# Optimization experiments

Hardware: AMD Instinct MI355X
Metric: run time of the kernel (lower is better)

Reference implementation:

```python
import jax, jax.numpy as jnp
import numpy as np

B, N, M = 2, 4096, 12288
K, SH, H, GK, NC, F = 64, 32, 64, 8, 200, 1


def sph_to_cart(theta, phi):
    st = jnp.sin(theta)
    return jnp.stack([st * jnp.cos(phi), st * jnp.sin(phi), jnp.cos(theta)], axis=-1)


def setup_inputs() -> dict:
    key = jax.random.key(0)
    ks = jax.random.split(key, 16)
    theta = jax.random.uniform(ks[0], (B, N)) * jnp.pi
    phi = jax.random.uniform(ks[1], (B, N)) * 2 * jnp.pi
    feat = jax.random.normal(ks[2], (B, N))
    xxx = jnp.stack([theta, phi, feat], axis=1)  # [B,3,N]
    pt = jax.random.uniform(ks[3], (M,)) * jnp.pi
    pp = jax.random.uniform(ks[4], (M,)) * 2 * jnp.pi
    pix_theta_phi = jnp.stack([pt, pp], axis=1)  # [M,2]
    s = 0.1
    return dict(
        xxx=xxx,
        pix_theta_phi=pix_theta_phi,
        att_w1=jax.random.normal(ks[5], (F + 1, SH)) * s,
        att_b1=jnp.zeros((SH,)),
        att_w2=jax.random.normal(ks[6], (SH, 1)) * s,
        att_b2=jnp.zeros((1,)),
        proj_w=jax.random.normal(ks[7], (F, H)) * s,
        proj_b=jnp.zeros((H,)),
        rel_w=jax.random.normal(ks[8], (3, H, H)) * s,
        rel_b=jnp.zeros((3, H)),
        root_w=jax.random.normal(ks[9], (3, H, H)) * s,
        out_w1=jax.random.normal(ks[10], (H, H)) * s,
        out_b1=jnp.zeros((H,)),
        out_w2=jax.random.normal(ks[11], (H, NC)) * s,
        out_b2=jnp.zeros((NC,)),
    )


def reference(xxx, pix_theta_phi, att_w1, att_b1, att_w2, att_b2, proj_w, proj_b,
              rel_w, rel_b, root_w, out_w1, out_b1, out_w2, out_b2):
    # --- sparse healpix sampler ---
    los_tp = jnp.transpose(xxx[:, :2, :], (0, 2, 1))   # [B,N,2]
    x = xxx[:, 2, :][..., None]                        # [B,N,1]
    r_los = sph_to_cart(los_tp[..., 0], los_tp[..., 1])           # [B,N,3]
    r_pix = sph_to_cart(pix_theta_phi[:, 0], pix_theta_phi[:, 1])  # [M,3]
    cos = jnp.clip(jnp.einsum('bnc,mc->bmn', r_los, r_pix), -1.0, 1.0)  # [B,M,N]
    vals, idx = jax.lax.top_k(cos, K)                  # [B,M,K]
    x_g = jax.vmap(lambda xb, ib: xb[ib])(x, idx)      # [B,M,K,F]
    d = jnp.arccos(jnp.clip(vals, -1.0, 1.0))          # [B,M,K]
    feat = jnp.concatenate([x_g, d[..., None]], axis=-1)  # [B,M,K,F+1]
    logits = jax.nn.relu(feat @ att_w1 + att_b1) @ att_w2 + att_b2  # [B,M,K,1]
    w = jax.nn.softmax(logits[..., 0], axis=-1)        # [B,M,K]
    pooled = jnp.einsum('bmk,bmkf->bmf', w, x_g)       # [B,M,F]
    # --- GNN on healpix grid ---
    h = jax.nn.relu(pooled @ proj_w + proj_b)          # [B,M,H]
    m = r_pix.shape[0]
    sq = jnp.sum(r_pix * r_pix, axis=1)
    d2 = sq[:, None] + sq[None, :] - 2.0 * (r_pix @ r_pix.T)       # [M,M]
    d2 = jnp.where(jnp.eye(m, dtype=bool), jnp.inf, d2)  # loop=False
    _, nbr = jax.lax.top_k(-d2, GK)                    # [M,GK] knn_graph
    for i in range(rel_w.shape[0]):
        agg = h[:, nbr, :].sum(axis=2)                 # sum-aggregate neighbor msgs
        h = jax.nn.relu(agg @ rel_w[i] + rel_b[i] + h @ root_w[i])
    graph_feat = h.mean(axis=1)                        # global_mean_pool -> [B,H]
    out = jax.nn.relu(graph_feat @ out_w1 + out_b1) @ out_w2 + out_b2
    return out
```

## Files before the change

### kernel.cpp

```cpp
#include <hip/hip_runtime.h>
#include <hip/hip_bf16.h>

#define B_ 2
#define N_ 4096
#define M_ 12288
#define K_ 64
#define SH_ 32
#define H_ 64
#define GK_ 8
#define NC_ 200

#define KCAP 128
#define BCAP2 48
#define MG_ 0.01f
#define C256_ 81.48733086f

static __device__ __forceinline__ unsigned f2key(float f) {
  unsigned b = __float_as_uint(f);
  return (b & 0x80000000u) ? ~b : (b | 0x80000000u);
}
static __device__ __forceinline__ float key2f(unsigned u) {
  unsigned b = (u & 0x80000000u) ? (u & 0x7fffffffu) : ~u;
  return __uint_as_float(b);
}
static __device__ __forceinline__ unsigned long long shflxor64(unsigned long long x, int m) {
  unsigned lo = (unsigned)x, hi = (unsigned)(x >> 32);
  lo = (unsigned)__shfl_xor((int)lo, m);
  hi = (unsigned)__shfl_xor((int)hi, m);
  return ((unsigned long long)hi << 32) | lo;
}
static __device__ __forceinline__ unsigned long long kpack(float s, int j) {
  return ((unsigned long long)f2key(s) << 14) | (unsigned)(16383 - j);
}
static __device__ __forceinline__ unsigned long long spack(float c, int n) {
  return ((unsigned long long)f2key(c) << 12) | (unsigned)(4095 - n);
}
static __device__ __forceinline__ int thbkt(float th) {
  int b = (int)(th * C256_);
  return b < 0 ? 0 : (b > 255 ? 255 : b);
}
static __device__ __forceinline__ float clamp1(float x) { return fminf(1.f, fmaxf(-1.f, x)); }
static __device__ __forceinline__ float rdlane(float v, int c) {
  return __uint_as_float((unsigned)__builtin_amdgcn_readlane((int)__float_as_uint(v), c));
}

__global__ __launch_bounds__(256) void sentinel_vE(float* out, int n, float val) {
  int t = blockIdx.x * 256 + threadIdx.x;
  if (t < n) out[t] = val;
}

#define GRIDB_ 129
#define PREPN_ (M_ + B_*N_ + B_*H_)
#define PREPB_ ((PREPN_ + 255)/256)

__global__ __launch_bounds__(256) void prep_vE(
    const float* __restrict__ xxx, const float* __restrict__ pix,
    float4* __restrict__ r_pix, float4* __restrict__ r_los, float* __restrict__ gf,
    float* __restrict__ kthrG, float* __restrict__ cthrG, unsigned* __restrict__ cnt)
{
  const float PI = 3.14159265358979f;
  if ((int)blockIdx.x < GRIDB_) {
    int gid  = blockIdx.x*4 + (threadIdx.x >> 6);
    if (gid >= 514) return;
    int lane = threadIdx.x & 63;
    int tgt  = (gid >= 257) ? 1 : 0;
    int gp   = gid - tgt*257;
    float thp = (float)gp * (PI/256.f);
    float cp = cosf(thp), sp = fmaxf(sinf(thp), 1e-6f);
    float thq = ((float)lane + 0.5f) * (PI/64.f);
    float sq = sinf(thq), cq = cosf(thq);
    float rinv = 1.0f / (sq * sp);
    float At = tgt ? (2.f*PI*PI*128.f/(float)N_) : (2.f*PI*PI*48.f/(float)M_);
    float lo = 1e-3f, hi = 3.1414f;
    for (int it = 0; it < 12; ++it) {
      float al = 0.5f*(lo + hi);
      float ca = cosf(al);
      float arg = clamp1((ca - cq*cp) * rinv);
      float ax = fabsf(arg);
      float ac = sqrtf(fmaxf(0.f, 1.f - ax)) *
                 fmaf(ax, fmaf(ax, fmaf(ax, -0.0187293f, 0.0742610f), -0.2121144f), 1.5707288f);
      ac = (arg < 0.f) ? (PI - ac) : ac;
      float S = ac;
      #pragma unroll
      for (int off = 32; off; off >>= 1) S += __shfl_xor(S, off);
      float A = 2.f * S * (PI/64.f);
      if (A < At) lo = al; else hi = al;
    }
    if (lane == 0) {
      float chv = cosf(hi);
      if (tgt) cthrG[gp] = chv - 1e-5f;
      else     kthrG[gp] = 2.f*chv - 1.00002f;
    }
  } else {
    int tid = ((int)blockIdx.x - GRIDB_)*256 + threadIdx.x;
    if (tid < M_) {
      float th = pix[2*tid], ph = pix[2*tid+1];
      float st = sinf(th);
      float x = st*cosf(ph), y = st*sinf(ph), z = cosf(th);
      r_pix[tid] = make_float4(x, y, z, x*x + y*y + z*z);
      atomicAdd(&cnt[thbkt(th)], 1u);
    }
    int t2 = tid - M_;
    if (t2 >= 0 && t2 < B_*N_) {
      int b = t2 >> 12, n = t2 & (N_-1);
      const float* xb = xxx + b*3*N_;
      float th = xb[n], ph = xb[N_+n], ft = xb[2*N_+n];
      float st = sinf(th);
      r_los[t2] = make_float4(st*cosf(ph), st*sinf(ph), cosf(th), ft);
      atomicAdd(&cnt[256 + b*256 + thbkt(th)], 1u);
    }
    int t3 = tid - M_ - B_*N_;
    if (t3 >= 0 && t3 < B_*H_) gf[t3] = 0.0f;
  }
}

__global__ __launch_bounds__(256) void scan_vE(
    const unsigned* __restrict__ cnt, int* __restrict__ pstart, int* __restrict__ lstart,
    unsigned* __restrict__ pcur, unsigned* __restrict__ lcur)
{
  __shared__ unsigned buf[256];
  const int t = threadIdx.x;
  for (int arr = 0; arr < 3; ++arr) {
    unsigned v = cnt[arr*256 + t];
    buf[t] = v;
    __syncthreads();
    for (int off = 1; off < 256; off <<= 1) {
      unsigned o = (t >= off) ? buf[t - off] : 0u;
      __syncthreads();
      buf[t] += o;
      __syncthreads();
    }
    unsigned incl = buf[t], excl = incl - v;
    if (arr == 0) {
      pstart[t] = (int)excl; if (t == 255) pstart[256] = (int)incl;
      pcur[t] = excl;
    } else {
      int b = arr - 1;
      lstart[b*257 + t] = (int)excl; if (t == 255) lstart[b*257 + 256] = (int)incl;
      lcur[b*256 + t] = excl;
    }
    __syncthreads();
  }
}

__global__ __launch_bounds__(256) void scatter_vE(
    const float* __restrict__ xxx, const float* __restrict__ pix,
    const float4* __restrict__ r_pix, const float4* __restrict__ r_los,
    unsigned* __restrict__ pcur, unsigned* __restrict__ lcur,
    float4* __restrict__ spix, int* __restrict__ sjdx,
    float4* __restrict__ slos, int* __restrict__ sldx)
{
  int tid = blockIdx.x * 256 + threadIdx.x;
  if (tid < M_) {
    int bkt = thbkt(pix[2*tid]);
    unsigned pos = atomicAdd(&pcur[bkt], 1u);
    spix[pos] = r_pix[tid];
    sjdx[pos] = tid;
  } else {
    int t2 = tid - M_;
    if (t2 < B_*N_) {
      int b = t2 >> 12, n = t2 & (N_-1);
      int bkt = thbkt(xxx[b*3*N_ + n]);
      unsigned pos = atomicAdd(&lcur[b*256 + bkt], 1u);
      slos[b*N_ + pos] = r_los[t2];
      sldx[b*N_ + pos] = n;
    }
  }
}

__global__ __launch_bounds__(512) void sampler_vE(
    const float* __restrict__ pix,
    const float4* __restrict__ spix, const int* __restrict__ sjdx,
    const float4* __restrict__ slos, const int* __restrict__ sldx,
    const int* __restrict__ lstart, const float4* __restrict__ r_los,
    const float* __restrict__ cthrG,
    const float* __restrict__ aw1, const float* __restrict__ ab1,
    const float* __restrict__ aw2, const float* __restrict__ ab2,
    float* __restrict__ pooled)
{
  __shared__ unsigned long long selKey[16][K_];
  __shared__ unsigned long long bndK[16][BCAP2];
  __shared__ unsigned hist[16][64];

  const int tid = threadIdx.x, wv = tid >> 6, lane = tid & 63;
  const int b  = blockIdx.y;
  const int srow0 = blockIdx.x*16 + wv*2, srow1 = srow0 + 1;
  const int r0 = wv*2, r1 = r0 + 1;
  const int m0 = sjdx[srow0], m1 = sjdx[srow1];
  const float4 p0 = spix[srow0], p1 = spix[srow1];
  const float thp0 = pix[2*m0], thp1 = pix[2*m1];
  const int g0 = thbkt(thp0), g1 = thbkt(thp1);
  const float th0 = fminf(cthrG[g0], cthrG[g0+1]);
  const float th1 = fminf(cthrG[g1], cthrG[g1+1]);
  const float inv0 = 63.999f / (1.000001f - th0);
  const float inv1 = 63.999f / (1.000001f - th1);
  const float4* sl = slos + b * N_;
  const int* sx = sldx + b * N_;
  const float4* rl = r_los + b * N_;
  const int* ls = lstart + b * 257;
  const unsigned long long ltm = (1ull << lane) - 1ull;

  hist[r0][lane] = 0u; hist[r1][lane] = 0u;

  int jlo, jhi;
  {
    float al0 = acosf(clamp1(th0)), al1 = acosf(clamp1(th1));
    int blo = thbkt(fminf(thp0 - al0, thp1 - al1) - MG_);
    int bhi = thbkt(fmaxf(thp0 + al0, thp1 + al1) + MG_);
    jlo = ls[blo]; jhi = ls[bhi + 1];
  }

  unsigned cnt0 = 0, cnt1 = 0;
  for (int base = jlo; base < jhi; base += 64) {
    int pos = base + lane;
    bool act = pos < jhi;
    float c0 = -2.f, c1 = -2.f;
    if (act) {
      float4 v = sl[pos];
      c0 = clamp1(v.x*p0.x + v.y*p0.y + v.z*p0.z);
      c1 = clamp1(v.x*p1.x + v.y*p1.y + v.z*p1.z);
    }
    bool pr0 = c0 > th0, pr1 = c1 > th1;
    if (pr0) atomicAdd(&hist[r0][(int)((c0 - th0) * inv0)], 1u);
    if (pr1) atomicAdd(&hist[r1][(int)((c1 - th1) * inv1)], 1u);
    cnt0 += (unsigned)__popcll(__ballot(pr0));
    cnt1 += (unsigned)__popcll(__ballot(pr1));
  }

  bool ok[2] = { cnt0 >= K_, cnt1 >= K_ };
  int tsel[2]; unsigned chi_[2], need_[2];
  for (int rr = 0; rr < 2; ++rr) {
    tsel[rr] = 64; chi_[rr] = 0; need_[rr] = 0;
    if (ok[rr]) {
      const int r = (rr == 0) ? r0 : r1;
      unsigned g = hist[r][lane], s = g;
      #pragma unroll
      for (int off = 1; off < 64; off <<= 1) {
        unsigned t2 = (unsigned)__shfl_down((int)s, off);
        s += (lane + off < 64) ? t2 : 0u;
      }
      unsigned snext = s - g;
      unsigned packed = (s >= K_ && snext < K_) ? (((unsigned)(lane+1) << 16) | snext) : 0u;
      #pragma unroll
      for (int off = 32; off; off >>= 1) {
        unsigned o = (unsigned)__shfl_xor((int)packed, off);
        packed = packed > o ? packed : o;
      }
      tsel[rr] = (int)(packed >> 16) - 1;
      chi_[rr] = packed & 0xFFFFu;
      need_[rr] = K_ - chi_[rr];
    }
  }

  bool done[2] = { false, false };
  if (ok[0] || ok[1]) {
    unsigned hiC0 = 0, bdC0 = 0, hiC1 = 0, bdC1 = 0;
    for (int base = jlo; base < jhi; base += 64) {
      int pos = base + lane;
      bool act = pos < jhi;
      float c0 = -2.f, c1 = -2.f; int n = 0;
      if (act) {
        float4 v = sl[pos]; n = sx[pos];
        c0 = clamp1(v.x*p0.x + v.y*p0.y + v.z*p0.z);
        c1 = clamp1(v.x*p1.x + v.y*p1.y + v.z*p1.z);
      }
      if (ok[0]) {
        int bin = (act && c0 > th0) ? (int)((c0 - th0) * inv0) : -1;
        bool pHi = bin > tsel[0], pBd = bin == tsel[0];
        unsigned long long mH = __ballot(pHi);
        unsigned offH = (unsigned)__popcll(mH & ltm);
        if (pHi && hiC0 + offH < K_) selKey[r0][hiC0 + offH] = spack(c0, n);
        hiC0 += (unsigned)__popcll(mH);
        unsigned long long mB = __ballot(pBd);
        unsigned offB = (unsigned)__popcll(mB & ltm);
        if (pBd && bdC0 + offB < BCAP2) bndK[r0][bdC0 + offB] = spack(c0, n);
        bdC0 += (unsigned)__popcll(mB);
      }
      if (ok[1]) {
        int bin = (act && c1 > th1) ? (int)((c1 - th1) * inv1) : -1;
        bool pHi = bin > tsel[1], pBd = bin == tsel[1];
        unsigned long long mH = __ballot(pHi);
        unsigned offH = (unsigned)__popcll(mH & ltm);
        if (pHi && hiC1 + offH < K_) selKey[r1][hiC1 + offH] = spack(c1, n);
        hiC1 += (unsigned)__popcll(mH);
        unsigned long long mB = __ballot(pBd);
        unsigned offB = (unsigned)__popcll(mB & ltm);
        if (pBd && bdC1 + offB < BCAP2) bndK[r1][bdC1 + offB] = spack(c1, n);
        bdC1 += (unsigned)__popcll(mB);
      }
    }
    for (int rr = 0; rr < 2; ++rr) {
      if (!ok[rr]) continue;
      unsigned bdC = (rr == 0) ? bdC0 : bdC1;
      const int r = (rr == 0) ? r0 : r1;
      if (bdC <= (unsigned)BCAP2) {
        if (lane < (int)bdC) {
          unsigned long long ki = bndK[r][lane];
          int rank = 0;
          for (int j = 0; j < (int)bdC; ++j) rank += (bndK[r][j] > ki) ? 1 : 0;
          if ((unsigned)rank < need_[rr]) selKey[r][chi_[rr] + rank] = ki;
        }
        done[rr] = true;
      }
    }
  }

  for (int rr = 0; rr < 2; ++rr) {
    const int r = (rr == 0) ? r0 : r1;
    const int m = (rr == 0) ? m0 : m1;
    const float4 p = (rr == 0) ? p0 : p1;
    const float thp = (rr == 0) ? thp0 : thp1;

    if (!done[rr]) {
      float th = (rr == 0) ? th0 : th1;
      float inv = (rr == 0) ? inv0 : inv1;
      unsigned cn = (rr == 0) ? cnt0 : cnt1;
      int wlo = jlo, whi = jhi;

      int tries = 0;
      while (cn < K_ && tries < 3) {
        th = 1.f - 1.6f*(1.f - th); ++tries;
        inv = 63.999f / (1.000001f - th);
        float al = acosf(clamp1(th));
        int blo = thbkt(thp - al - MG_), bhi = thbkt(thp + al + MG_);
        wlo = ls[blo]; whi = ls[bhi + 1];
        hist[r][lane] = 0u;
        cn = 0;
        for (int base = wlo; base < whi; base += 64) {
          int pos = base + lane;
          bool act = pos < whi;
          float c = -2.f;
          if (act) {
            float4 v = sl[pos];
            c = clamp1(v.x*p.x + v.y*p.y + v.z*p.z);
          }
          bool pr = c > th;
          if (pr) atomicAdd(&hist[r][(int)((c - th) * inv)], 1u);
          cn += (unsigned)__popcll(__ballot(pr));
        }
      }

      bool fin = false;
      if (cn >= K_) {
        unsigned g = hist[r][lane], s = g;
        #pragma unroll
        for (int off = 1; off < 64; off <<= 1) {
          unsigned t2 = (unsigned)__shfl_down((int)s, off);
          s += (lane + off < 64) ? t2 : 0u;
        }
        unsigned snext = s - g;
        unsigned packed = (s >= K_ && snext < K_) ? (((unsigned)(lane+1) << 16) | snext) : 0u;
        #pragma unroll
        for (int off = 32; off; off >>= 1) {
          unsigned o = (unsigned)__shfl_xor((int)packed, off);
          packed = packed > o ? packed : o;
        }
        const int t = (int)(packed >> 16) - 1;
        const unsigned chi = packed & 0xFFFFu;
        const unsigned need = K_ - chi;

        unsigned hiC = 0, bdC = 0;
        for (int base = wlo; base < whi; base += 64) {
          int pos = base + lane;
          bool act = pos < whi;
          float c = -2.f; int n = 0;
          if (act) {
            float4 v = sl[pos]; n = sx[pos];
            c = clamp1(v.x*p.x + v.y*p.y + v.z*p.z);
          }
          int bin = (act && c > th) ? (int)((c - th) * inv) : -1;
          bool pHi = bin > t;
          bool pBd = bin == t;
          unsigned long long mH = __ballot(pHi);
          unsigned offH = (unsigned)__popcll(mH & ltm);
          if (pHi && hiC + offH < K_) selKey[r][hiC + offH] = spack(c, n);
          hiC += (unsigned)__popcll(mH);
          unsigned long long mB = __ballot(pBd);
          unsigned offB = (unsigned)__popcll(mB & ltm);
          if (pBd && bdC + offB < BCAP2) bndK[r][bdC + offB] = spack(c, n);
          bdC += (unsigned)__popcll(mB);
        }
        if (bdC <= (unsigned)BCAP2) {
          if (lane < (int)bdC) {
            unsigned long long ki = bndK[r][lane];
            int rank = 0;
            for (int j = 0; j < (int)bdC; ++j) rank += (bndK[r][j] > ki) ? 1 : 0;
            if ((unsigned)rank < need) selKey[r][chi + rank] = ki;
          }
          fin = true;
        }
      }

      if (!fin) {
        unsigned long long prev = ~0ull;
        for (int rd = 0; rd < K_; ++rd) {
          unsigned long long best = 0ull;
          for (int i = 0; i < 64; ++i) {
            int n = lane + 64*i;
            float4 v = rl[n];
            float c = clamp1(v.x*p.x + v.y*p.y + v.z*p.z);
            unsigned long long k = spack(c, n);
            if (k < prev && k > best) best = k;
          }
          #pragma unroll
          for (int off = 1; off < 64; off <<= 1) {
            unsigned long long o = shflxor64(best, off);
            best = o > best ? o : best;
          }
          if (lane == 0) selKey[r][rd] = best;
          prev = best;
        }
      }
    }

    {
      unsigned long long key = selKey[r][lane];
      int n = 4095 - (int)(key & 0xFFFull);
      float c = key2f((unsigned)(key >> 12));
      float xg = rl[n].w;
      float d  = acosf(clamp1(c));
      float acc = ab2[0];
      for (int s2 = 0; s2 < SH_; ++s2)
        acc += fmaxf(xg*aw1[s2] + d*aw1[SH_+s2] + ab1[s2], 0.f) * aw2[s2];
      float mx = acc;
      #pragma unroll
      for (int off = 32; off; off >>= 1) mx = fmaxf(mx, __shfl_xor(mx, off));
      float e = expf(acc - mx);
      float se = e, sxe = e * xg;
      #pragma unroll
      for (int off = 32; off; off >>= 1) { se += __shfl_xor(se, off); sxe += __shfl_xor(sxe, off); }
      if (lane == 0) pooled[b*M_ + m] = sxe / se;
    }
  }
}

__global__ __launch_bounds__(512) void knn_vE(
    const float* __restrict__ pix,
    const float4* __restrict__ spix, const int* __restrict__ sjdx,
    const int* __restrict__ pstart, const float4* __restrict__ r_pix,
    const float* __restrict__ kthrG, int* __restrict__ nbr)
{
  __shared__ unsigned long long cKey[16][KCAP];

  const int tid = threadIdx.x, wv = tid >> 6, lane = tid & 63;
  const int lr0 = wv*2;
  const int srow0 = blockIdx.x*16 + lr0, srow1 = srow0 + 1;
  const int i0 = sjdx[srow0], i1 = sjdx[srow1];
  const float4 p0 = spix[srow0], p1 = spix[srow1];
  const float thp0 = pix[2*i0], thp1 = pix[2*i1];
  const int g0 = thbkt(thp0), g1 = thbkt(thp1);
  const float t0 = fminf(kthrG[g0], kthrG[g0+1]);
  const float t1 = fminf(kthrG[g1], kthrG[g1+1]);
  const unsigned long long ltm = (1ull << lane) - 1ull;

  unsigned cnt0 = 0, cnt1 = 0;
  {
    float al0 = acosf(clamp1((t0 + 1.00002f)*0.5f));
    float al1 = acosf(clamp1((t1 + 1.00002f)*0.5f));
    int blo = thbkt(fminf(thp0 - al0, thp1 - al1) - MG_);
    int bhi = thbkt(fmaxf(thp0 + al0, thp1 + al1) + MG_);
    int jlo = pstart[blo], jhi = pstart[bhi + 1];
    for (int base = jlo; base < jhi; base += 64) {
      int pos = base + lane;
      bool act = pos < jhi;
      float s0 = -1e30f, s1 = -1e30f; int j = -1;
      if (act) {
        float4 v = spix[pos]; j = sjdx[pos];
        s0 = 2.f*(p0.x*v.x + p0.y*v.y + p0.z*v.z) - v.w;
        s1 = 2.f*(p1.x*v.x + p1.y*v.y + p1.z*v.z) - v.w;
      }
      bool pr0 = act && (j != i0) && (s0 > t0);
      bool pr1 = act && (j != i1) && (s1 > t1);
      unsigned long long mk0 = __ballot(pr0);
      if (mk0) {
        unsigned off = (unsigned)__popcll(mk0 & ltm);
        if (pr0 && cnt0 + off < KCAP) cKey[lr0][cnt0 + off] = kpack(s0, j);
        cnt0 += (unsigned)__popcll(mk0);
      }
      unsigned long long mk1 = __ballot(pr1);
      if (mk1) {
        unsigned off = (unsigned)__popcll(mk1 & ltm);
        if (pr1 && cnt1 + off < KCAP) cKey[lr0+1][cnt1 + off] = kpack(s1, j);
        cnt1 += (unsigned)__popcll(mk1);
      }
    }
  }

  for (int rr = 0; rr < 2; ++rr) {
    const int lr = lr0 + rr;
    const int i  = (rr == 0) ? i0 : i1;
    const float4 pi = (rr == 0) ? p0 : p1;
    const float thp = (rr == 0) ? thp0 : thp1;
    float th = (rr == 0) ? t0 : t1;
    unsigned cn = (rr == 0) ? cnt0 : cnt1;

    int tries = 0;
    while (cn < (unsigned)GK_ && tries < 3) {
      th = 1.6f*th - 0.6f; ++tries;
      float al = acosf(clamp1((th + 1.00002f)*0.5f));
      int blo = thbkt(thp - al - MG_), bhi = thbkt(thp + al + MG_);
      int jlo = pstart[blo], jhi = pstart[bhi + 1];
      cn = 0;
      for (int base = jlo; base < jhi; base += 64) {
        int pos = base + lane;
        bool act = pos < jhi;
        float s = -1e30f; int j = -1;
        if (act) {
          float4 v = spix[pos]; j = sjdx[pos];
          s = 2.f*(pi.x*v.x + pi.y*v.y + pi.z*v.z) - v.w;
        }
        bool pr = act && (j != i) && (s > th);
        unsigned long long mk = __ballot(pr);
        if (mk) {
          unsigned off = (unsigned)__popcll(mk & ltm);
          if (pr && cn + off < KCAP) cKey[lr][cn + off] = kpack(s, j);
          cn += (unsigned)__popcll(mk);
        }
      }
    }

    if (cn >= (unsigned)GK_ && cn <= (unsigned)KCAP) {
      unsigned long long pk[2];
      #pragma unroll
      for (int t2 = 0; t2 < 2; ++t2) {
        int idx = lane + 64*t2;
        pk[t2] = (idx < (int)cn) ? cKey[lr][idx] : 0ull;
      }
      for (int round = 0; round < GK_; ++round) {
        unsigned long long loc = pk[0]; int lt = 0;
        if (pk[1] > loc) { loc = pk[1]; lt = 1; }
        unsigned long long best = loc;
        #pragma unroll
        for (int off = 1; off < 64; off <<= 1) {
          unsigned long long o = shflxor64(best, off);
          best = o > best ? o : best;
        }
        if (loc == best) pk[lt] = 0ull;
        if (lane == round) nbr[i*GK_ + round] = 16383 - (int)(best & 16383ull);
      }
    } else {
      unsigned long long prev = ~0ull;
      for (int rd = 0; rd < GK_; ++rd) {
        unsigned long long best = 0ull;
        for (int j = lane; j < M_; j += 64) {
          float4 v = r_pix[j];
          float s = 2.f*(pi.x*v.x + pi.y*v.y + pi.z*v.z) - v.w;
          if (j != i) {
            unsigned long long k = kpack(s, j);
            if (k < prev && k > best) best = k;
          }
        }
        #pragma unroll
        for (int off = 1; off < 64; off <<= 1) {
          unsigned long long o = shflxor64(best, off);
          best = o > best ? o : best;
        }
        if (lane == rd) nbr[i*GK_ + rd] = 16383 - (int)(best & 16383ull);
        prev = best;
      }
    }
  }
}

__global__ __launch_bounds__(256) void gnn1f_vE(
    const float* __restrict__ pooled, float* __restrict__ hout, const int* __restrict__ nbr,
    const float* __restrict__ pw, const float* __restrict__ pb,
    const float* __restrict__ relw, const float* __restrict__ relb,
    const float* __restrict__ rootw)
{
  __shared__ float wrel[H_*H_], wroot[H_*H_];
  const int tid = threadIdx.x;
  #pragma unroll
  for (int q = 0; q < 16; ++q) {
    int idx = tid + 256*q;
    wrel[idx]  = relw[idx];
    wroot[idx] = rootw[idx];
  }
  __syncthreads();

  const int lane = tid & 63;
  const int wave = tid >> 6;
  const int b = blockIdx.y;
  const int m0 = blockIdx.x * 16 + wave * 4;
  const float* pldb = pooled + (size_t)b * M_;
  const float pwl = pw[lane], pbl = pb[lane], rbl = relb[lane];

  float h[4], agg[4], acc[4];
  #pragma unroll
  for (int t = 0; t < 4; ++t) {
    int m = m0 + t;
    float ps = pldb[m];
    h[t] = fmaxf(ps*pwl + pbl, 0.f);
    float a = 0.f;
    #pragma unroll
    for (int k = 0; k < GK_; ++k) {
      int nb = nbr[m*GK_ + k];
      nb = nb < 0 ? 0 : (nb >= M_ ? M_-1 : nb);
      float pn = pldb[nb];
      a += fmaxf(pn*pwl + pbl, 0.f);
    }
    agg[t] = a;
    acc[t] = rbl;
  }
  #pragma unroll
  for (int c = 0; c < H_; ++c) {
    float wr = wrel[c*H_ + lane], wo = wroot[c*H_ + lane];
    #pragma unroll
    for (int t = 0; t < 4; ++t)
      acc[t] += rdlane(agg[t], c) * wr + rdlane(h[t], c) * wo;
  }
  #pragma unroll
  for (int t = 0; t < 4; ++t)
    hout[((size_t)b*M_ + m0 + t)*H_ + lane] = fmaxf(acc[t], 0.f);
}

__global__ __launch_bounds__(256) void gnn_vE(
    const float* __restrict__ hin, float* __restrict__ hout, const int* __restrict__ nbr,
    const float* __restrict__ relw, const float* __restrict__ relb,
    const float* __restrict__ rootw)
{
  __shared__ float wrel[H_*H_], wroot[H_*H_];
  const int tid = threadIdx.x;
  #pragma unroll
  for (int q = 0; q < 16; ++q) {
    int idx = tid + 256*q;
    wrel[idx]  = relw[idx];
    wroot[idx] = rootw[idx];
  }
  __syncthreads();

  const int lane = tid & 63;
  const int wave = tid >> 6;
  const int b = blockIdx.y;
  const int m0 = blockIdx.x * 16 + wave * 4;
  const float* hb = hin + (size_t)b * M_ * H_;
  const float rbl = relb[lane];

  float h[4], agg[4], acc[4];
  #pragma unroll
  for (int t = 0; t < 4; ++t) {
    int m = m0 + t;
    h[t] = hb[m*H_ + lane];
    float a = 0.f;
    #pragma unroll
    for (int k = 0; k < GK_; ++k) {
      int nb = nbr[m*GK_ + k];
      nb = nb < 0 ? 0 : (nb >= M_ ? M_-1 : nb);
      a += hb[nb*H_ + lane];
    }
    agg[t] = a;
    acc[t] = rbl;
  }
  #pragma unroll
  for (int c = 0; c < H_; ++c) {
    float wr = wrel[c*H_ + lane], wo = wroot[c*H_ + lane];
    #pragma unroll
    for (int t = 0; t < 4; ++t)
      acc[t] += rdlane(agg[t], c) * wr + rdlane(h[t], c) * wo;
  }
  #pragma unroll
  for (int t = 0; t < 4; ++t)
    hout[((size_t)b*M_ + m0 + t)*H_ + lane] = fmaxf(acc[t], 0.f);
}

__global__ __launch_bounds__(256) void gnn3r_vE(
    const float* __restrict__ hin, float* __restrict__ gf, const int* __restrict__ nbr,
    const float* __restrict__ relw, const float* __restrict__ relb,
    const float* __restrict__ rootw)
{
  __shared__ float wrel[H_*H_], wroot[H_*H_];
  __shared__ float gacc[H_];
  const int tid = threadIdx.x;
  #pragma unroll
  for (int q = 0; q < 16; ++q) {
    int idx = tid + 256*q;
    wrel[idx]  = relw[idx];
    wroot[idx] = rootw[idx];
  }
  if (tid < H_) gacc[tid] = 0.f;
  __syncthreads();

  const int lane = tid & 63;
  const int wave = tid >> 6;
  const int b = blockIdx.y;
  const int m0 = blockIdx.x * 16 + wave * 4;
  const float* hb = hin + (size_t)b * M_ * H_;
  const float rbl = relb[lane];

  float h[4], agg[4], acc[4];
  #pragma unroll
  for (int t = 0; t < 4; ++t) {
    int m = m0 + t;
    h[t] = hb[m*H_ + lane];
    float a = 0.f;
    #pragma unroll
    for (int k = 0; k < GK_; ++k) {
      int nb = nbr[m*GK_ + k];
      nb = nb < 0 ? 0 : (nb >= M_ ? M_-1 : nb);
      a += hb[nb*H_ + lane];
    }
    agg[t] = a;
    acc[t] = rbl;
  }
  #pragma unroll
  for (int c = 0; c < H_; ++c) {
    float wr = wrel[c*H_ + lane], wo = wroot[c*H_ + lane];
    #pragma unroll
    for (int t = 0; t < 4; ++t)
      acc[t] += rdlane(agg[t], c) * wr + rdlane(h[t], c) * wo;
  }
  float ps = fmaxf(acc[0], 0.f) + fmaxf(acc[1], 0.f) + fmaxf(acc[2], 0.f) + fmaxf(acc[3], 0.f);
  atomicAdd(&gacc[lane], ps);
  __syncthreads();
  if (tid < H_) atomicAdd(&gf[b*H_ + tid], gacc[tid]);
}

__global__ __launch_bounds__(256) void head_vE(
    const float* __restrict__ gf, const float* __restrict__ w1,
    const float* __restrict__ b1, const float* __restrict__ w2,
    const float* __restrict__ b2, float* __restrict__ out)
{
  __shared__ float gfm[B_][H_], hid[B_][H_];
  const int tid = threadIdx.x;
  if (tid < B_*H_) gfm[tid >> 6][tid & 63] = gf[tid] * (1.f / (float)M_);
  __syncthreads();
  if (tid < B_*H_) {
    int b = tid >> 6, j = tid & 63;
    float acc = b1[j];
    for (int c = 0; c < H_; ++c) acc += gfm[b][c] * w1[c*H_ + j];
    hid[b][j] = fmaxf(acc, 0.f);
  }
  __syncthreads();
  for (int t = tid; t < B_*NC_; t += 256) {
    int b = t / NC_, o = t - b*NC_;
    float acc = b2[o];
    for (int j = 0; j < H_; ++j) acc += hid[b][j] * w2[j*NC_ + o];
    out[t] = acc;
  }
}

extern "C" void kernel_launch(void* const* d_in, const int* in_sizes, int n_in,
                              void* d_out, int out_size, void* d_ws, size_t ws_size,
                              hipStream_t stream)
{
  float* out = (float*)d_out;

  const size_t need = (size_t)M_*16 + (size_t)B_*N_*16 + (size_t)B_*M_*4
                    + (size_t)M_*GK_*4 + 2*(size_t)B_*M_*H_*4 + (size_t)B_*H_*4;
  bool ok_ws = ws_size >= need;
  bool ok_in = (n_in == 15) && (out_size == B_*NC_)
            && in_sizes[0] == B_*3*N_ && in_sizes[1] == M_*2
            && in_sizes[2] == 2*SH_ && in_sizes[5] == 1
            && in_sizes[8] == 3*H_*H_ && in_sizes[13] == H_*NC_;
  if (!ok_ws || !ok_in) {
    sentinel_vE<<<(out_size + 255)/256, 256, 0, stream>>>(out, out_size, ok_in ? 42.f : 43.f);
    return;
  }

  const float* xxx    = (const float*)d_in[0];
  const float* pix    = (const float*)d_in[1];
  const float* att_w1 = (const float*)d_in[2];
  const float* att_b1 = (const float*)d_in[3];
  const float* att_w2 = (const float*)d_in[4];
  const float* att_b2 = (const float*)d_in[5];
  const float* proj_w = (const float*)d_in[6];
  const float* proj_b = (const float*)d_in[7];
  const float* rel_w  = (const float*)d_in[8];
  const float* rel_b  = (const float*)d_in[9];
  const float* root_w = (const float*)d_in[10];
  const float* out_w1 = (const float*)d_in[11];
  const float* out_b1 = (const float*)d_in[12];
  const float* out_w2 = (const float*)d_in[13];
  const float* out_b2 = (const float*)d_in[14];

  char* w = (char*)d_ws;
  float4* r_pix = (float4*)w;  w += (size_t)M_ * 16;
  float4* r_los = (float4*)w;  w += (size_t)B_ * N_ * 16;
  float*  pooled = (float*)w;  w += (size_t)B_ * M_ * 4;
  int*    nbr = (int*)w;       w += (size_t)M_ * GK_ * 4;
  float*  h0 = (float*)w;      w += (size_t)B_ * M_ * H_ * 4;
  float*  h1 = (float*)w;      w += (size_t)B_ * M_ * H_ * 4;
  float*  gf = (float*)w;      w += (size_t)B_ * H_ * 4;

  float*  kthrG = h0;
  float*  cthrG = h0 + 512;
  float4* spix = (float4*)(h0 + 2*M_);
  int*    sjdx = (int*)(h0 + 6*M_);
  float4* slos = (float4*)(h0 + 7*M_);
  int*    sldx = (int*)(h0 + 7*M_ + 4*B_*N_);
  unsigned* cnt = (unsigned*)(h0 + 7*M_ + 5*B_*N_);
  int*    pstart = (int*)(cnt + 768);
  int*    lstart = pstart + 257;
  unsigned* pcur = (unsigned*)(lstart + 514);
  unsigned* lcur = pcur + 256;

  hipMemsetAsync(cnt, 0, 768*sizeof(unsigned), stream);
  prep_vE<<<GRIDB_ + PREPB_, 256, 0, stream>>>(xxx, pix, r_pix, r_los, gf, kthrG, cthrG, cnt);
  scan_vE<<<1, 256, 0, stream>>>(cnt, pstart, lstart, pcur, lcur);
  scatter_vE<<<(M_ + B_*N_ + 255)/256, 256, 0, stream>>>(xxx, pix, r_pix, r_los, pcur, lcur,
                                                         spix, sjdx, slos, sldx);
  sampler_vE<<<dim3(M_/16, B_), 512, 0, stream>>>(pix, spix, sjdx, slos, sldx, lstart, r_los,
                                                  cthrG, att_w1, att_b1, att_w2, att_b2, pooled);
  knn_vE<<<M_/16, 512, 0, stream>>>(pix, spix, sjdx, pstart, r_pix, kthrG, nbr);
  gnn1f_vE<<<dim3(M_/16, B_), 256, 0, stream>>>(pooled, h1, nbr, proj_w, proj_b,
                                                rel_w + 0*H_*H_, rel_b + 0*H_, root_w + 0*H_*H_);
  gnn_vE<<<dim3(M_/16, B_), 256, 0, stream>>>(h1, h0, nbr, rel_w + 1*H_*H_, rel_b + 1*H_, root_w + 1*H_*H_);
  gnn3r_vE<<<dim3(M_/16, B_), 256, 0, stream>>>(h0, gf, nbr, rel_w + 2*H_*H_, rel_b + 2*H_, root_w + 2*H_*H_);
  head_vE<<<1, 256, 0, stream>>>(gf, out_w1, out_b1, out_w2, out_b2, out);
}
```

Baseline: 254.4 us.

## Cache above-threshold sampler candidates in LDS to avoid second global scan

The sampler's first pass now stores packed (cosine, index) keys for candidates above the threshold into a per-row shared-memory buffer of up to 192 entries. The histogram and the high/boundary selection are then built from that buffer, so the second pass over the sorted line-of-sight points (global loads plus dot products) is skipped. When the candidate count exceeds the buffer, the code falls back to a rescan. In exchange, shared memory per block grows by about 24 KB, which may lower occupancy, and the first pass now also loads indices.

```diff
diff --git a/kernel.cpp b/kernel.cpp
--- a/kernel.cpp
+++ b/kernel.cpp
@@ -12,6 +12,7 @@
 
 #define KCAP 128
 #define BCAP2 48
+#define SCAP 192
 #define MG_ 0.01f
 #define C256_ 81.48733086f
 
@@ -44,7 +45,7 @@
   return __uint_as_float((unsigned)__builtin_amdgcn_readlane((int)__float_as_uint(v), c));
 }
 
-__global__ __launch_bounds__(256) void sentinel_vE(float* out, int n, float val) {
+__global__ __launch_bounds__(256) void sentinel_vF(float* out, int n, float val) {
   int t = blockIdx.x * 256 + threadIdx.x;
   if (t < n) out[t] = val;
 }
@@ -53,7 +54,7 @@
 #define PREPN_ (M_ + B_*N_ + B_*H_)
 #define PREPB_ ((PREPN_ + 255)/256)
 
-__global__ __launch_bounds__(256) void prep_vE(
+__global__ __launch_bounds__(256) void prep_vF(
     const float* __restrict__ xxx, const float* __restrict__ pix,
     float4* __restrict__ r_pix, float4* __restrict__ r_los, float* __restrict__ gf,
     float* __restrict__ kthrG, float* __restrict__ cthrG, unsigned* __restrict__ cnt)
@@ -114,7 +115,7 @@
   }
 }
 
-__global__ __launch_bounds__(256) void scan_vE(
+__global__ __launch_bounds__(256) void scan_vF(
     const unsigned* __restrict__ cnt, int* __restrict__ pstart, int* __restrict__ lstart,
     unsigned* __restrict__ pcur, unsigned* __restrict__ lcur)
 {
@@ -143,7 +144,7 @@
   }
 }
 
-__global__ __launch_bounds__(256) void scatter_vE(
+__global__ __launch_bounds__(256) void scatter_vF(
     const float* __restrict__ xxx, const float* __restrict__ pix,
     const float4* __restrict__ r_pix, const float4* __restrict__ r_los,
     unsigned* __restrict__ pcur, unsigned* __restrict__ lcur,
@@ -168,7 +169,7 @@
   }
 }
 
-__global__ __launch_bounds__(512) void sampler_vE(
+__global__ __launch_bounds__(512) void sampler_vF(
     const float* __restrict__ pix,
     const float4* __restrict__ spix, const int* __restrict__ sjdx,
     const float4* __restrict__ slos, const int* __restrict__ sldx,
@@ -178,6 +179,7 @@
     const float* __restrict__ aw2, const float* __restrict__ ab2,
     float* __restrict__ pooled)
 {
+  __shared__ unsigned long long cand[16][SCAP];
   __shared__ unsigned long long selKey[16][K_];
   __shared__ unsigned long long bndK[16][BCAP2];
   __shared__ unsigned hist[16][64];
@@ -200,8 +202,6 @@
   const int* ls = lstart + b * 257;
   const unsigned long long ltm = (1ull << lane) - 1ull;
 
-  hist[r0][lane] = 0u; hist[r1][lane] = 0u;
-
   int jlo, jhi;
   {
     float al0 = acosf(clamp1(th0)), al1 = acosf(clamp1(th1));
@@ -214,25 +214,43 @@
   for (int base = jlo; base < jhi; base += 64) {
     int pos = base + lane;
     bool act = pos < jhi;
-    float c0 = -2.f, c1 = -2.f;
+    float c0 = -2.f, c1 = -2.f; int n = 0;
     if (act) {
-      float4 v = sl[pos];
+      float4 v = sl[pos]; n = sx[pos];
       c0 = clamp1(v.x*p0.x + v.y*p0.y + v.z*p0.z);
       c1 = clamp1(v.x*p1.x + v.y*p1.y + v.z*p1.z);
     }
     bool pr0 = c0 > th0, pr1 = c1 > th1;
-    if (pr0) atomicAdd(&hist[r0][(int)((c0 - th0) * inv0)], 1u);
-    if (pr1) atomicAdd(&hist[r1][(int)((c1 - th1) * inv1)], 1u);
-    cnt0 += (unsigned)__popcll(__ballot(pr0));
-    cnt1 += (unsigned)__popcll(__ballot(pr1));
-  }
-
-  bool ok[2] = { cnt0 >= K_, cnt1 >= K_ };
-  int tsel[2]; unsigned chi_[2], need_[2];
+    unsigned long long mk0 = __ballot(pr0);
+    if (mk0) {
+      unsigned off = (unsigned)__popcll(mk0 & ltm);
+      if (pr0 && cnt0 + off < SCAP) cand[r0][cnt0 + off] = spack(c0, n);
+      cnt0 += (unsigned)__popcll(mk0);
+    }
+    unsigned long long mk1 = __ballot(pr1);
+    if (mk1) {
+      unsigned off = (unsigned)__popcll(mk1 & ltm);
+      if (pr1 && cnt1 + off < SCAP) cand[r1][cnt1 + off] = spack(c1, n);
+      cnt1 += (unsigned)__popcll(mk1);
+    }
+  }
+
   for (int rr = 0; rr < 2; ++rr) {
-    tsel[rr] = 64; chi_[rr] = 0; need_[rr] = 0;
-    if (ok[rr]) {
-      const int r = (rr == 0) ? r0 : r1;
+    const int r = (rr == 0) ? r0 : r1;
+    const int m = (rr == 0) ? m0 : m1;
+    const float4 p = (rr == 0) ? p0 : p1;
+    const float thp = (rr == 0) ? thp0 : thp1;
+    const float thg = (rr == 0) ? th0 : th1;
+    const float invg = (rr == 0) ? inv0 : inv1;
+    unsigned cn = (rr == 0) ? cnt0 : cnt1;
+    bool fin = false;
+
+    if (cn >= (unsigned)K_ && cn <= (unsigned)SCAP) {
+      hist[r][lane] = 0u;
+      for (int i = lane; i < (int)cn; i += 64) {
+        float c = key2f((unsigned)(cand[r][i] >> 12));
+        atomicAdd(&hist[r][(int)((c - thg) * invg)], 1u);
+      }
       unsigned g = hist[r][lane], s = g;
       #pragma unroll
       for (int off = 1; off < 64; off <<= 1) {
@@ -246,76 +264,59 @@
         unsigned o = (unsigned)__shfl_xor((int)packed, off);
         packed = packed > o ? packed : o;
       }
-      tsel[rr] = (int)(packed >> 16) - 1;
-      chi_[rr] = packed & 0xFFFFu;
-      need_[rr] = K_ - chi_[rr];
-    }
-  }
-
-  bool done[2] = { false, false };
-  if (ok[0] || ok[1]) {
-    unsigned hiC0 = 0, bdC0 = 0, hiC1 = 0, bdC1 = 0;
-    for (int base = jlo; base < jhi; base += 64) {
-      int pos = base + lane;
-      bool act = pos < jhi;
-      float c0 = -2.f, c1 = -2.f; int n = 0;
-      if (act) {
-        float4 v = sl[pos]; n = sx[pos];
-        c0 = clamp1(v.x*p0.x + v.y*p0.y + v.z*p0.z);
-        c1 = clamp1(v.x*p1.x + v.y*p1.y + v.z*p1.z);
-      }
-      if (ok[0]) {
-        int bin = (act && c0 > th0) ? (int)((c0 - th0) * inv0) : -1;
-        bool pHi = bin > tsel[0], pBd = bin == tsel[0];
+      const int t = (int)(packed >> 16) - 1;
+      const unsigned chi = packed & 0xFFFFu;
+      const unsigned need = K_ - chi;
+
+      unsigned hiC = 0, bdC = 0;
+      for (int i0 = 0; i0 < (int)cn; i0 += 64) {
+        int i = i0 + lane;
+        bool act = i < (int)cn;
+        unsigned long long key = act ? cand[r][i] : 0ull;
+        int bin = -1;
+        if (act) bin = (int)((key2f((unsigned)(key >> 12)) - thg) * invg);
+        bool pHi = act && bin > t, pBd = act && bin == t;
         unsigned long long mH = __ballot(pHi);
         unsigned offH = (unsigned)__popcll(mH & ltm);
-        if (pHi && hiC0 + offH < K_) selKey[r0][hiC0 + offH] = spack(c0, n);
-        hiC0 += (unsigned)__popcll(mH);
+        if (pHi && hiC + offH < K_) selKey[r][hiC + offH] = key;
+        hiC += (unsigned)__popcll(mH);
         unsigned long long mB = __ballot(pBd);
         unsigned offB = (unsigned)__popcll(mB & ltm);
-        if (pBd && bdC0 + offB < BCAP2) bndK[r0][bdC0 + offB] = spack(c0, n);
-        bdC0 += (unsigned)__popcll(mB);
-      }
-      if (ok[1]) {
-        int bin = (act && c1 > th1) ? (int)((c1 - th1) * inv1) : -1;
-        bool pHi = bin > tsel[1], pBd = bin == tsel[1];
-        unsigned long long mH = __ballot(pHi);
-        unsigned offH = (unsigned)__popcll(mH & ltm);
-        if (pHi && hiC1 + offH < K_) selKey[r1][hiC1 + offH] = spack(c1, n);
-        hiC1 += (unsigned)__popcll(mH);
-        unsigned long long mB = __ballot(pBd);
-        unsigned offB = (unsigned)__popcll(mB & ltm);
-        if (pBd && bdC1 + offB < BCAP2) bndK[r1][bdC1 + offB] = spack(c1, n);
-        bdC1 += (unsigned)__popcll(mB);
-      }
-    }
-    for (int rr = 0; rr < 2; ++rr) {
-      if (!ok[rr]) continue;
-      unsigned bdC = (rr == 0) ? bdC0 : bdC1;
-      const int r = (rr == 0) ? r0 : r1;
+        if (pBd && bdC + offB < BCAP2) bndK[r][bdC + offB] = key;
+        bdC += (unsigned)__popcll(mB);
+      }
       if (bdC <= (unsigned)BCAP2) {
         if (lane < (int)bdC) {
           unsigned long long ki = bndK[r][lane];
           int rank = 0;
           for (int j = 0; j < (int)bdC; ++j) rank += (bndK[r][j] > ki) ? 1 : 0;
-          if ((unsigned)rank < need_[rr]) selKey[r][chi_[rr] + rank] = ki;
-        }
-        done[rr] = true;
-      }
-    }
-  }
-
-  for (int rr = 0; rr < 2; ++rr) {
-    const int r = (rr == 0) ? r0 : r1;
-    const int m = (rr == 0) ? m0 : m1;
-    const float4 p = (rr == 0) ? p0 : p1;
-    const float thp = (rr == 0) ? thp0 : thp1;
-
-    if (!done[rr]) {
-      float th = (rr == 0) ? th0 : th1;
-      float inv = (rr == 0) ? inv0 : inv1;
-      unsigned cn = (rr == 0) ? cnt0 : cnt1;
+          if ((unsigned)rank < need) selKey[r][chi + rank] = ki;
+        }
+        fin = true;
+      }
+    }
+
+    if (!fin) {
+      float th = thg;
+      float inv = invg;
       int wlo = jlo, whi = jhi;
+
+      if (cn >= (unsigned)K_) {
+        hist[r][lane] = 0u;
+        cn = 0;
+        for (int base = wlo; base < whi; base += 64) {
+          int pos = base + lane;
+          bool act = pos < whi;
+          float c = -2.f;
+          if (act) {
+            float4 v = sl[pos];
+            c = clamp1(v.x*p.x + v.y*p.y + v.z*p.z);
+          }
+          bool pr = c > th;
+          if (pr) atomicAdd(&hist[r][(int)((c - th) * inv)], 1u);
+          cn += (unsigned)__popcll(__ballot(pr));
+        }
+      }
 
       int tries = 0;
       while (cn < K_ && tries < 3) {
@@ -340,7 +341,7 @@
         }
       }
 
-      bool fin = false;
+      bool fin2 = false;
       if (cn >= K_) {
         unsigned g = hist[r][lane], s = g;
         #pragma unroll
@@ -387,11 +388,11 @@
             for (int j = 0; j < (int)bdC; ++j) rank += (bndK[r][j] > ki) ? 1 : 0;
             if ((unsigned)rank < need) selKey[r][chi + rank] = ki;
           }
-          fin = true;
-        }
-      }
-
-      if (!fin) {
+          fin2 = true;
+        }
+      }
+
+      if (!fin2) {
         unsigned long long prev = ~0ull;
         for (int rd = 0; rd < K_; ++rd) {
           unsigned long long best = 0ull;
@@ -434,7 +435,7 @@
   }
 }
 
-__global__ __launch_bounds__(512) void knn_vE(
+__global__ __launch_bounds__(512) void knn_vF(
     const float* __restrict__ pix,
     const float4* __restrict__ spix, const int* __restrict__ sjdx,
     const int* __restrict__ pstart, const float4* __restrict__ r_pix,
@@ -562,7 +563,7 @@
   }
 }
 
-__global__ __launch_bounds__(256) void gnn1f_vE(
+__global__ __launch_bounds__(256) void gnn1f_vF(
     const float* __restrict__ pooled, float* __restrict__ hout, const int* __restrict__ nbr,
     const float* __restrict__ pw, const float* __restrict__ pb,
     const float* __restrict__ relw, const float* __restrict__ relb,
@@ -614,7 +615,7 @@
     hout[((size_t)b*M_ + m0 + t)*H_ + lane] = fmaxf(acc[t], 0.f);
 }
 
-__global__ __launch_bounds__(256) void gnn_vE(
+__global__ __launch_bounds__(256) void gnn_vF(
     const float* __restrict__ hin, float* __restrict__ hout, const int* __restrict__ nbr,
     const float* __restrict__ relw, const float* __restrict__ relb,
     const float* __restrict__ rootw)
@@ -663,7 +664,7 @@
     hout[((size_t)b*M_ + m0 + t)*H_ + lane] = fmaxf(acc[t], 0.f);
 }
 
-__global__ __launch_bounds__(256) void gnn3r_vE(
+__global__ __launch_bounds__(256) void gnn3r_vF(
     const float* __restrict__ hin, float* __restrict__ gf, const int* __restrict__ nbr,
     const float* __restrict__ relw, const float* __restrict__ relb,
     const float* __restrict__ rootw)
@@ -715,7 +716,7 @@
   if (tid < H_) atomicAdd(&gf[b*H_ + tid], gacc[tid]);
 }
 
-__global__ __launch_bounds__(256) void head_vE(
+__global__ __launch_bounds__(256) void head_vF(
     const float* __restrict__ gf, const float* __restrict__ w1,
     const float* __restrict__ b1, const float* __restrict__ w2,
     const float* __restrict__ b2, float* __restrict__ out)
@@ -753,7 +754,7 @@
             && in_sizes[2] == 2*SH_ && in_sizes[5] == 1
             && in_sizes[8] == 3*H_*H_ && in_sizes[13] == H_*NC_;
   if (!ok_ws || !ok_in) {
-    sentinel_vE<<<(out_size + 255)/256, 256, 0, stream>>>(out, out_size, ok_in ? 42.f : 43.f);
+    sentinel_vF<<<(out_size + 255)/256, 256, 0, stream>>>(out, out_size, ok_in ? 42.f : 43.f);
     return;
   }
 
@@ -795,16 +796,16 @@
   unsigned* lcur = pcur + 256;
 
   hipMemsetAsync(cnt, 0, 768*sizeof(unsigned), stream);
-  prep_vE<<<GRIDB_ + PREPB_, 256, 0, stream>>>(xxx, pix, r_pix, r_los, gf, kthrG, cthrG, cnt);
-  scan_vE<<<1, 256, 0, stream>>>(cnt, pstart, lstart, pcur, lcur);
-  scatter_vE<<<(M_ + B_*N_ + 255)/256, 256, 0, stream>>>(xxx, pix, r_pix, r_los, pcur, lcur,
+  prep_vF<<<GRIDB_ + PREPB_, 256, 0, stream>>>(xxx, pix, r_pix, r_los, gf, kthrG, cthrG, cnt);
+  scan_vF<<<1, 256, 0, stream>>>(cnt, pstart, lstart, pcur, lcur);
+  scatter_vF<<<(M_ + B_*N_ + 255)/256, 256, 0, stream>>>(xxx, pix, r_pix, r_los, pcur, lcur,
                                                          spix, sjdx, slos, sldx);
-  sampler_vE<<<dim3(M_/16, B_), 512, 0, stream>>>(pix, spix, sjdx, slos, sldx, lstart, r_los,
+  sampler_vF<<<dim3(M_/16, B_), 512, 0, stream>>>(pix, spix, sjdx, slos, sldx, lstart, r_los,
                                                   cthrG, att_w1, att_b1, att_w2, att_b2, pooled);
-  knn_vE<<<M_/16, 512, 0, stream>>>(pix, spix, sjdx, pstart, r_pix, kthrG, nbr);
-  gnn1f_vE<<<dim3(M_/16, B_), 256, 0, stream>>>(pooled, h1, nbr, proj_w, proj_b,
+  knn_vF<<<M_/16, 512, 0, stream>>>(pix, spix, sjdx, pstart, r_pix, kthrG, nbr);
+  gnn1f_vF<<<dim3(M_/16, B_), 256, 0, stream>>>(pooled, h1, nbr, proj_w, proj_b,
                                                 rel_w + 0*H_*H_, rel_b + 0*H_, root_w + 0*H_*H_);
-  gnn_vE<<<dim3(M_/16, B_), 256, 0, stream>>>(h1, h0, nbr, rel_w + 1*H_*H_, rel_b + 1*H_, root_w + 1*H_*H_);
-  gnn3r_vE<<<dim3(M_/16, B_), 256, 0, stream>>>(h0, gf, nbr, rel_w + 2*H_*H_, rel_b + 2*H_, root_w + 2*H_*H_);
-  head_vE<<<1, 256, 0, stream>>>(gf, out_w1, out_b1, out_w2, out_b2, out);
-}
+  gnn_vF<<<dim3(M_/16, B_), 256, 0, stream>>>(h1, h0, nbr, rel_w + 1*H_*H_, rel_b + 1*H_, root_w + 1*H_*H_);
+  gnn3r_vF<<<dim3(M_/16, B_), 256, 0, stream>>>(h0, gf, nbr, rel_w + 2*H_*H_, rel_b + 2*H_, root_w + 2*H_*H_);
+  head_vF<<<1, 256, 0, stream>>>(gf, out_w1, out_b1, out_w2, out_b2, out);
+}
```

Result: faster. 239.2 us (-6.0%).
